# Kernel tuning notes

Hardware: AMD Instinct MI355X
Metric: run time of the kernel (lower is better)

## Reference

```python
import jax, jax.numpy as jnp
import numpy as np

D_MODEL = 2048
D_INNER = 4096
D_CONV = 4
D_STATE = 16
DT_RANK = 128  # (d_model + 15) // 16
EPS = 1e-5
B_SZ, SEQ = 2, 2048


def _silu(x):
    return x * jax.nn.sigmoid(x)


def setup_inputs() -> dict:
    key = jax.random.key(0)
    ks = jax.random.split(key, 10)
    s = lambda k, shape, sc=0.02: jax.random.normal(k, shape, jnp.float32) * sc
    # S4D-real init for A_log, small negative bias for dt (standard Mamba init)
    A_log = jnp.log(jnp.tile(jnp.arange(1, D_STATE + 1, dtype=jnp.float32), (D_INNER, 1)))
    return {
        "hidden_states": jax.random.normal(ks[0], (B_SZ, SEQ, D_MODEL), jnp.float32),
        "norm_scale": jnp.ones((D_MODEL,), jnp.float32),
        "in_proj_w": s(ks[1], (2 * D_INNER, D_MODEL)),
        "conv_w": s(ks[2], (D_INNER, 1, D_CONV), 0.1),
        "conv_b": s(ks[3], (D_INNER,), 0.1),
        "x_proj_w": s(ks[4], (DT_RANK + 2 * D_STATE, D_INNER)),
        "dt_proj_w": s(ks[5], (D_INNER, DT_RANK), 0.1),
        "dt_proj_b": jnp.full((D_INNER,), -4.0, jnp.float32) + s(ks[6], (D_INNER,), 0.1),
        "out_proj_w": s(ks[7], (D_MODEL, D_INNER)),
        "A_log": A_log,
        "D": jnp.ones((D_INNER,), jnp.float32),
    }


def reference(hidden_states, norm_scale, in_proj_w, conv_w, conv_b, x_proj_w,
              dt_proj_w, dt_proj_b, out_proj_w, A_log, D):
    B, L, _ = hidden_states.shape
    residual = hidden_states
    # RMSNorm
    rms = jnp.sqrt(jnp.mean(hidden_states ** 2, axis=-1, keepdims=True) + EPS)
    xn = hidden_states / rms * norm_scale
    # in_proj -> [B, L, 2*d_inner]; torch code keeps this as projected_states
    xz = jnp.einsum('bld,ed->ble', xn, in_proj_w)
    x_in = xz[..., :D_INNER].transpose(0, 2, 1)  # [B, d_inner, L]
    z = xz[..., D_INNER:]                        # [B, L, d_inner]
    # depthwise causal conv1d (padding d_conv-1, truncated to L) + SiLU
    xc = jax.lax.conv_general_dilated(
        x_in, conv_w, window_strides=(1,), padding=[(D_CONV - 1, 0)],
        feature_group_count=D_INNER)
    xc = _silu(xc + conv_b[None, :, None])       # [B, d_inner, L]
    # x_proj -> dt, B, C
    x_dbl = jnp.einsum('bdl,rd->brl', xc, x_proj_w)  # [B, dt_rank+2*d_state, L]
    dt_low = x_dbl[:, :DT_RANK]
    Bm = x_dbl[:, DT_RANK:DT_RANK + D_STATE]         # [B, d_state, L]
    Cm = x_dbl[:, DT_RANK + D_STATE:]                # [B, d_state, L]
    delta = jax.nn.softplus(
        jnp.einsum('dr,brl->bdl', dt_proj_w, dt_low) + dt_proj_b[None, :, None])
    A = -jnp.exp(A_log)                              # [d_inner, d_state]
    # selective scan: h_t = exp(delta_t * A) * h_{t-1} + delta_t * B_t * u_t
    delta_t = delta.transpose(2, 0, 1)  # [L, B, d_inner]
    u_t = xc.transpose(2, 0, 1)         # [L, B, d_inner]
    B_t = Bm.transpose(2, 0, 1)         # [L, B, d_state]
    C_t = Cm.transpose(2, 0, 1)         # [L, B, d_state]

    def step(h, inp):
        d_, b_, c_, u_ = inp
        dA = jnp.exp(d_[..., None] * A)                      # [B, d_inner, d_state]
        h = h * dA + (d_ * u_)[..., None] * b_[:, None, :]   # [B, d_inner, d_state]
        y = jnp.einsum('bds,bs->bd', h, c_)                  # [B, d_inner]
        return h, y

    h0 = jnp.zeros((B, D_INNER, D_STATE), hidden_states.dtype)
    _, ys = jax.lax.scan(step, h0, (delta_t, B_t, C_t, u_t))  # [L, B, d_inner]
    y = ys.transpose(1, 0, 2) + xc.transpose(0, 2, 1) * D     # [B, L, d_inner]
    y = y * _silu(z)
    out = jnp.einsum('bld,od->blo', y, out_proj_w)            # [B, L, d_model]
    return residual + out, xz
```

## Files before the change

### kernel.cpp

```cpp
#include <hip/hip_runtime.h>
#include <cstdint>
#include <cstddef>

#define DM   2048
#define DI   4096
#define DST  16
#define DTR  128
#define SEQL 2048
#define NTOK 4096
#define XZW  8192
#define NCHAIN 8192
#define CL   32
#define NCH  64

typedef short short8 __attribute__((ext_vector_type(8)));
typedef float f32x4 __attribute__((ext_vector_type(4)));

__device__ __forceinline__ short f2bf(float x) {
  union { float f; uint32_t u; } v; v.f = x;
  uint32_t r = v.u + 0x7fffu + ((v.u >> 16) & 1u);
  return (short)(r >> 16);
}
__device__ __forceinline__ float bf2f(short s) {
  union { uint32_t u; float f; } v; v.u = ((uint32_t)(uint16_t)s) << 16;
  return v.f;
}

__device__ __forceinline__ void stage16(const short* g, short* l) {
#if __has_builtin(__builtin_amdgcn_global_load_lds)
  __builtin_amdgcn_global_load_lds((const __attribute__((address_space(1))) void*)g,
                                   (__attribute__((address_space(3))) void*)l, 16, 0, 0);
#else
  *(short8*)l = *(const short8*)g;
#endif
}

__global__ __launch_bounds__(256) void cvt4_k(const float* __restrict__ in,
                                              short* __restrict__ out, int n4) {
  int i = blockIdx.x * 256 + threadIdx.x;
  if (i >= n4) return;
  float4 v = ((const float4*)in)[i];
  short4 o;
  o.x = f2bf(v.x); o.y = f2bf(v.y); o.z = f2bf(v.z); o.w = f2bf(v.w);
  ((short4*)out)[i] = o;
}

__global__ __launch_bounds__(256) void pad_xproj_k(const float* __restrict__ xp,
                                                   short* __restrict__ out) {
  int i = blockIdx.x * 256 + threadIdx.x;
  if (i >= 256 * 1024) return;
  int r = i >> 10;
  float4 v = make_float4(0.f, 0.f, 0.f, 0.f);
  if (r < 160) v = ((const float4*)xp)[i];
  short4 o;
  o.x = f2bf(v.x); o.y = f2bf(v.y); o.z = f2bf(v.z); o.w = f2bf(v.w);
  ((short4*)out)[i] = o;
}

__global__ __launch_bounds__(256) void rmsnorm_k(const float* __restrict__ hs,
                                                 const float* __restrict__ sc,
                                                 short* __restrict__ xn) {
  const int token = blockIdx.x;
  const int tid = threadIdx.x;
  const float* row = hs + (size_t)token * DM;
  float4 a = ((const float4*)row)[tid];
  float4 b = ((const float4*)row)[tid + 256];
  float ss = a.x*a.x + a.y*a.y + a.z*a.z + a.w*a.w
           + b.x*b.x + b.y*b.y + b.z*b.z + b.w*b.w;
  #pragma unroll
  for (int o = 32; o > 0; o >>= 1) ss += __shfl_xor(ss, o);
  __shared__ float wsum[4];
  if ((tid & 63) == 0) wsum[tid >> 6] = ss;
  __syncthreads();
  float tot = wsum[0] + wsum[1] + wsum[2] + wsum[3];
  float inv = rsqrtf(tot * (1.0f / DM) + 1e-5f);
  float4 s1 = ((const float4*)sc)[tid];
  float4 s2 = ((const float4*)sc)[tid + 256];
  short4 o1, o2;
  o1.x = f2bf(a.x * inv * s1.x); o1.y = f2bf(a.y * inv * s1.y);
  o1.z = f2bf(a.z * inv * s1.z); o1.w = f2bf(a.w * inv * s1.w);
  o2.x = f2bf(b.x * inv * s2.x); o2.y = f2bf(b.y * inv * s2.y);
  o2.z = f2bf(b.z * inv * s2.z); o2.w = f2bf(b.w * inv * s2.w);
  ((short4*)xn)[(size_t)token * (DM / 4) + tid] = o1;
  ((short4*)xn)[(size_t)token * (DM / 4) + tid + 256] = o2;
}

#define LGKM_FENCE() do { asm volatile("s_waitcnt lgkmcnt(0)" ::: "memory"); \
                          __builtin_amdgcn_sched_barrier(0); } while (0)

template <int RBY, int RBX>
__global__ __launch_bounds__(512) void gemm_big(const short* __restrict__ A,
                                                const short* __restrict__ B,
                                                int K, int ksz, int N, int nbx,
                                                float* __restrict__ out_f,
                                                size_t zstride) {
  constexpr int MFR = 8;
  constexpr int BM = 256;
  constexpr int ABYTES = BM * 128;
  constexpr int BBYTES = 256 * 128;
  constexpr int BUF = ABYTES + BBYTES;
  constexpr int FPP = 4;
  __shared__ char lds[2 * BUF];

  const int tid = threadIdx.x;
  const int lane = tid & 63;
  const int wid = tid >> 6;
  const int wm = wid >> 2;
  const int wn = wid & 3;
  const int lr = lane & 15;
  const int lj = lane >> 4;

  const int xcd = blockIdx.x & 7;
  const int idx = blockIdx.x >> 3;
  const int nrgx = nbx / RBX;
  const int by = (xcd / nrgx) * RBY + idx / RBX;
  const int bx = (xcd % nrgx) * RBX + idx % RBX;
  const size_t m0 = (size_t)by * BM;
  const size_t n0 = (size_t)bx * 256;

  const int kbase = blockIdx.y * ksz;
  out_f += (size_t)blockIdx.y * zstride;
  const int NT = ksz >> 6;

  auto stA1 = [&](int t, char* buf, int s) {
    const int k0 = kbase + (t << 6);
    const int off = s * 8192 + tid * 16;
    const int r = off >> 7;
    const int j = (off >> 4) & 7;
    stage16(A + (m0 + r) * (size_t)K + k0 + ((j ^ (r & 7)) << 3),
            (short*)(buf + off));
  };
  auto stB1 = [&](int t, char* buf, int s) {
    const int k0 = kbase + (t << 6);
    const int off = s * 8192 + tid * 16;
    const int r = off >> 7;
    const int j = (off >> 4) & 7;
    stage16(B + (n0 + r) * (size_t)K + k0 + ((j ^ (r & 7)) << 3),
            (short*)(buf + ABYTES + off));
  };

#define READ_A(dst, fbase)                                                   \
  _Pragma("unroll")                                                          \
  for (int f = 0; f < 4; ++f) {                                              \
    const int arow = wm * (BM / 2) + ((fbase) + f) * 16 + lr;                \
    _Pragma("unroll")                                                        \
    for (int ks = 0; ks < 2; ++ks)                                           \
      dst[f][ks] = *(const short8*)(cur + arow * 128 +                       \
                     ((((ks << 2) + lj) ^ (arow & 7)) << 4));                \
  }
#define READ_B(dst, gbase)                                                   \
  _Pragma("unroll")                                                          \
  for (int g = 0; g < 2; ++g) {                                              \
    const int brow = wn * 64 + ((gbase) + g) * 16 + lr;                      \
    _Pragma("unroll")                                                        \
    for (int ks = 0; ks < 2; ++ks)                                           \
      dst[g][ks] = *(const short8*)(cur + ABYTES + brow * 128 +              \
                     ((((ks << 2) + lj) ^ (brow & 7)) << 4));                \
  }
#define MFMA_Q(accoff, avoff, gbase, bvx)                                    \
  __builtin_amdgcn_s_setprio(1);                                             \
  _Pragma("unroll")                                                          \
  for (int ks = 0; ks < 2; ++ks)                                             \
    _Pragma("unroll")                                                        \
    for (int f = 0; f < FPP; ++f)                                            \
      _Pragma("unroll")                                                      \
      for (int g = 0; g < 2; ++g)                                            \
        acc[(accoff) + f][(gbase) + g] = __builtin_amdgcn_mfma_f32_16x16x32_bf16( \
            av[(avoff) + f][ks], bvx[g][ks], acc[(accoff) + f][(gbase) + g], 0, 0, 0); \
  __builtin_amdgcn_s_setprio(0);

  f32x4 acc[MFR][4] = {};

  {
    #pragma unroll
    for (int s = 0; s < 4; ++s) stA1(0, lds, s);
    #pragma unroll
    for (int s = 0; s < 4; ++s) stB1(0, lds, s);
    if (NT > 1) {
      stA1(1, lds + BUF, 0); stA1(1, lds + BUF, 2);
      asm volatile("s_waitcnt vmcnt(2)" ::: "memory");
    } else asm volatile("s_waitcnt vmcnt(0)" ::: "memory");
    __builtin_amdgcn_s_barrier();
    __builtin_amdgcn_sched_barrier(0);
  }

  for (int t = 0; t < NT; ++t) {
    char* cur = lds + (t & 1) * BUF;
    char* nxt = lds + ((t + 1) & 1) * BUF;
    const bool m1 = (t + 1) < NT;
    const bool m2 = (t + 2) < NT;
    short8 av[4][2], bv0[2][2], bv1[2][2];

    READ_A(av, 0);
    READ_B(bv0, 0);
    if (m1) { stA1(t + 1, nxt, 1); stA1(t + 1, nxt, 3); }
    LGKM_FENCE();
    MFMA_Q(0, 0, 0, bv0);
    __builtin_amdgcn_s_barrier();

    READ_B(bv1, 2);
    if (m1) { stB1(t + 1, nxt, 0); stB1(t + 1, nxt, 1); }
    LGKM_FENCE();
    MFMA_Q(0, 0, 2, bv1);
    __builtin_amdgcn_s_barrier();

    READ_A(av, 4);
    if (m1) { stB1(t + 1, nxt, 2); stB1(t + 1, nxt, 3); }
    if (m2) { stA1(t + 2, cur, 0); stA1(t + 2, cur, 2); }
    LGKM_FENCE();
    MFMA_Q(4, 0, 2, bv1);
    __builtin_amdgcn_s_barrier();

    MFMA_Q(4, 0, 0, bv0);
    if (m2) asm volatile("s_waitcnt vmcnt(2)" ::: "memory");
    else    asm volatile("s_waitcnt vmcnt(0)" ::: "memory");
    __builtin_amdgcn_s_barrier();
    __builtin_amdgcn_sched_barrier(0);
  }

  #pragma unroll
  for (int f = 0; f < MFR; ++f)
    #pragma unroll
    for (int g = 0; g < 4; ++g)
      #pragma unroll
      for (int jj = 0; jj < 4; ++jj) {
        const size_t row = m0 + wm * (BM / 2) + f * 16 + lj * 4 + jj;
        const size_t col = n0 + wn * 64 + g * 16 + lr;
        out_f[row * (size_t)N + col] = acc[f][g][jj];
      }
#undef READ_A
#undef READ_B
#undef MFMA_Q
}

__global__ __launch_bounds__(256) void combine_k(const float* __restrict__ part,
                                                 const float* __restrict__ hs,
                                                 float* __restrict__ out0) {
  const size_t i = (size_t)blockIdx.x * 256 + threadIdx.x;
  const float4 p0 = ((const float4*)part)[i];
  const float4 p1 = ((const float4*)part)[i + (size_t)NTOK * DM / 4];
  const float4 r  = ((const float4*)hs)[i];
  float4 o;
  o.x = r.x + p0.x + p1.x; o.y = r.y + p0.y + p1.y;
  o.z = r.z + p0.z + p1.z; o.w = r.w + p0.w + p1.w;
  ((float4*)out0)[i] = o;
}

template <int EPI>
__global__ __launch_bounds__(256) void gemm_nt(const short* __restrict__ A,
                                               const short* __restrict__ B,
                                               int ld, int K, int N,
                                               float* __restrict__ out_f,
                                               const float* __restrict__ aux_f,
                                               short* __restrict__ out_bf) {
  __shared__ short As[128 * 64];
  __shared__ short Bs[128 * 64];
  const int tid = threadIdx.x;
  const int lane = tid & 63;
  const int wid = tid >> 6;
  const int wr = wid >> 1, wc = wid & 1;
  const size_t m0 = (size_t)blockIdx.y * 128;
  const size_t n0 = (size_t)blockIdx.x * 128;
  A += (size_t)blockIdx.z * K;
  B += (size_t)blockIdx.z * K;
  f32x4 acc[4][4] = {};
  for (int k0 = 0; k0 < K; k0 += 64) {
    #pragma unroll
    for (int i = 0; i < 4; ++i) {
      const int off = i * 4096 + tid * 16;
      const int r = off >> 7;
      const int ke = (off & 127) >> 1;
      stage16(A + (m0 + r) * (size_t)ld + k0 + ke, &As[off >> 1]);
      stage16(B + (n0 + r) * (size_t)ld + k0 + ke, &Bs[off >> 1]);
    }
    __syncthreads();
    #pragma unroll
    for (int kk = 0; kk < 64; kk += 32) {
      short8 af[4], bfr[4];
      const int kb = kk + (lane >> 4) * 8;
      const int rr = lane & 15;
      #pragma unroll
      for (int f = 0; f < 4; ++f) {
        af[f]  = *(const short8*)&As[(wr * 64 + f * 16 + rr) * 64 + kb];
        bfr[f] = *(const short8*)&Bs[(wc * 64 + f * 16 + rr) * 64 + kb];
      }
      #pragma unroll
      for (int fm = 0; fm < 4; ++fm)
        #pragma unroll
        for (int fn = 0; fn < 4; ++fn)
          acc[fm][fn] = __builtin_amdgcn_mfma_f32_16x16x32_bf16(af[fm], bfr[fn], acc[fm][fn], 0, 0, 0);
    }
    __syncthreads();
  }
  const int rbase = (lane >> 4) * 4;
  const int cbase = lane & 15;
  #pragma unroll
  for (int fm = 0; fm < 4; ++fm) {
    #pragma unroll
    for (int fn = 0; fn < 4; ++fn) {
      #pragma unroll
      for (int j = 0; j < 4; ++j) {
        const size_t row = m0 + wr * 64 + fm * 16 + rbase + j;
        const size_t col = n0 + wc * 64 + fn * 16 + cbase;
        const float v = acc[fm][fn][j];
        if constexpr (EPI == 2) {
          float x = v + aux_f[col];
          float sp = (x > 20.f) ? x : log1pf(__expf(x));
          out_bf[row * (size_t)N + col] = f2bf(sp);
        } else {
          if (col < 160)
            out_f[((size_t)blockIdx.z * NTOK + row) * (size_t)N + col] = v;
        }
      }
    }
  }
}

__global__ __launch_bounds__(256) void xdbl_epi_k(const float* __restrict__ part,
                                                  short* __restrict__ dtl,
                                                  float* __restrict__ Bc,
                                                  float* __restrict__ Cc) {
  const int row = blockIdx.x;
  const int col = threadIdx.x;
  if (col >= 160) return;
  const size_t i = (size_t)row * 256 + col;
  const float v = part[i] + part[(size_t)NTOK * 256 + i]
                + part[(size_t)2 * NTOK * 256 + i]
                + part[(size_t)3 * NTOK * 256 + i];
  if (col < 128)      dtl[(size_t)row * 128 + col] = f2bf(v);
  else if (col < 144) Bc[(size_t)row * 16 + (col - 128)] = v;
  else                Cc[(size_t)row * 16 + (col - 144)] = v;
}

__global__ __launch_bounds__(256) void conv_silu_k(const float* __restrict__ xz,
                                                   const float* __restrict__ cw,
                                                   const float* __restrict__ cb,
                                                   short* __restrict__ xc) {
  const int d = blockIdx.x * 256 + threadIdx.x;
  const int t0 = blockIdx.y * 8;
  const int l0 = t0 & (SEQL - 1);
  const float4 w = ((const float4*)cw)[d];
  const float bias = cb[d];
  float x0 = (l0 >= 3) ? xz[(size_t)(t0 - 3) * XZW + d] : 0.f;
  float x1 = (l0 >= 2) ? xz[(size_t)(t0 - 2) * XZW + d] : 0.f;
  float x2 = (l0 >= 1) ? xz[(size_t)(t0 - 1) * XZW + d] : 0.f;
  #pragma unroll
  for (int i = 0; i < 8; ++i) {
    const float x3 = xz[(size_t)(t0 + i) * XZW + d];
    const float acc = bias + w.x * x0 + w.y * x1 + w.z * x2 + w.w * x3;
    const float sv = acc / (1.f + __expf(-acc));
    xc[(size_t)(t0 + i) * DI + d] = f2bf(sv);
    x0 = x1; x1 = x2; x2 = x3;
  }
}

__global__ __launch_bounds__(256) void scan1_k(const short* __restrict__ del_bf,
                                               const short* __restrict__ xc,
                                               const float* __restrict__ Bc,
                                               const float* __restrict__ alog,
                                               float* __restrict__ hloc,
                                               float* __restrict__ Ssum) {
  const int t = blockIdx.x * 256 + threadIdx.x;
  const int sub = t & 1;
  const int chain = (t >> 1) & (NCHAIN - 1);
  const int chunk = t >> 14;
  const int b = chain >> 12;
  const int d = chain & 4095;
  float A[8];
  #pragma unroll
  for (int j = 0; j < 8; ++j) A[j] = -__expf(alog[d * 16 + sub * 8 + j]);
  float h[8] = {};
  float S = 0.f;
  size_t token = (size_t)b * SEQL + (size_t)chunk * CL;
  #pragma unroll 2
  for (int l = 0; l < CL; ++l, ++token) {
    const float delta = bf2f(del_bf[token * DI + d]);
    const float u = bf2f(xc[token * DI + d]);
    const float du = delta * u;
    S += delta;
    const float4 B0 = ((const float4*)Bc)[token * 4 + sub * 2];
    const float4 B1 = ((const float4*)Bc)[token * 4 + sub * 2 + 1];
    const float Bv[8] = {B0.x, B0.y, B0.z, B0.w, B1.x, B1.y, B1.z, B1.w};
    #pragma unroll
    for (int j = 0; j < 8; ++j)
      h[j] = h[j] * __expf(delta * A[j]) + du * Bv[j];
  }
  const size_t idx = (size_t)(chunk * NCHAIN + chain) * 4 + sub * 2;
  ((float4*)hloc)[idx]     = make_float4(h[0], h[1], h[2], h[3]);
  ((float4*)hloc)[idx + 1] = make_float4(h[4], h[5], h[6], h[7]);
  if (sub == 0) Ssum[chunk * NCHAIN + chain] = S;
}

__global__ __launch_bounds__(256) void scan2_k(float* __restrict__ hloc,
                                               const float* __restrict__ Ssum,
                                               const float* __restrict__ alog) {
  const int t = blockIdx.x * 256 + threadIdx.x;
  const int q = t & 3;
  const int chain = t >> 2;
  const int d = chain & 4095;
  float A[4];
  #pragma unroll
  for (int j = 0; j < 4; ++j) A[j] = -__expf(alog[d * 16 + q * 4 + j]);
  float4 h = make_float4(0.f, 0.f, 0.f, 0.f);
  for (int c = 0; c < NCH; ++c) {
    const size_t idx = (size_t)(c * NCHAIN + chain) * 4 + q;
    const float S = Ssum[c * NCHAIN + chain];
    const float4 hl = ((const float4*)hloc)[idx];
    ((float4*)hloc)[idx] = h;
    h.x = h.x * __expf(A[0] * S) + hl.x;
    h.y = h.y * __expf(A[1] * S) + hl.y;
    h.z = h.z * __expf(A[2] * S) + hl.z;
    h.w = h.w * __expf(A[3] * S) + hl.w;
  }
}

__global__ __launch_bounds__(256) void scan3_k(const short* __restrict__ del_bf,
                                               const short* __restrict__ xc,
                                               const float* __restrict__ Bc,
                                               const float* __restrict__ Cc,
                                               const float* __restrict__ xzbuf,
                                               const float* __restrict__ alog,
                                               const float* __restrict__ dvec,
                                               const float* __restrict__ hin,
                                               short* __restrict__ y) {
  const int t = blockIdx.x * 256 + threadIdx.x;
  const int sub = t & 1;
  const int chain = (t >> 1) & (NCHAIN - 1);
  const int chunk = t >> 14;
  const int b = chain >> 12;
  const int d = chain & 4095;
  float A[8];
  #pragma unroll
  for (int j = 0; j < 8; ++j) A[j] = -__expf(alog[d * 16 + sub * 8 + j]);
  const float Dd = dvec[d];
  const size_t idx = (size_t)(chunk * NCHAIN + chain) * 4 + sub * 2;
  const float4 h0 = ((const float4*)hin)[idx];
  const float4 h1 = ((const float4*)hin)[idx + 1];
  float h[8] = {h0.x, h0.y, h0.z, h0.w, h1.x, h1.y, h1.z, h1.w};
  size_t token = (size_t)b * SEQL + (size_t)chunk * CL;
  #pragma unroll 2
  for (int l = 0; l < CL; ++l, ++token) {
    const float delta = bf2f(del_bf[token * DI + d]);
    const float u = bf2f(xc[token * DI + d]);
    const float du = delta * u;
    const float4 B0 = ((const float4*)Bc)[token * 4 + sub * 2];
    const float4 B1 = ((const float4*)Bc)[token * 4 + sub * 2 + 1];
    const float4 C0 = ((const float4*)Cc)[token * 4 + sub * 2];
    const float4 C1 = ((const float4*)Cc)[token * 4 + sub * 2 + 1];
    const float Bv[8] = {B0.x, B0.y, B0.z, B0.w, B1.x, B1.y, B1.z, B1.w};
    const float Cv[8] = {C0.x, C0.y, C0.z, C0.w, C1.x, C1.y, C1.z, C1.w};
    float yp = 0.f;
    #pragma unroll
    for (int j = 0; j < 8; ++j) {
      h[j] = h[j] * __expf(delta * A[j]) + du * Bv[j];
      yp += h[j] * Cv[j];
    }
    yp += __shfl_xor(yp, 1);
    if (sub == 0) {
      const float z = xzbuf[token * XZW + DI + d];
      const float sz = z / (1.f + __expf(-z));
      y[token * DI + d] = f2bf((yp + u * Dd) * sz);
    }
  }
}

extern "C" void kernel_launch(void* const* d_in, const int* in_sizes, int n_in,
                              void* d_out, int out_size, void* d_ws, size_t ws_size,
                              hipStream_t stream) {
  const float* hs   = (const float*)d_in[0];
  const float* nsc  = (const float*)d_in[1];
  const float* win  = (const float*)d_in[2];
  const float* cw   = (const float*)d_in[3];
  const float* cb   = (const float*)d_in[4];
  const float* wxp  = (const float*)d_in[5];
  const float* wdt  = (const float*)d_in[6];
  const float* bdt  = (const float*)d_in[7];
  const float* wout = (const float*)d_in[8];
  const float* alog = (const float*)d_in[9];
  const float* dvec = (const float*)d_in[10];

  float* out0 = (float*)d_out;
  float* xz   = out0 + (size_t)NTOK * DM;

  char* w = (char*)d_ws;
  size_t off = 0;
  auto alloc = [&](size_t bytes) {
    char* p = w + off;
    off += (bytes + 255) & ~(size_t)255;
    return p;
  };
  short* xn_bf   = (short*)alloc((size_t)NTOK * DM * 2);
  short* win_bf  = (short*)alloc((size_t)XZW * DM * 2);
  short* wout_bf = (short*)alloc((size_t)DM * DI * 2);
  short* wdt_bf  = (short*)alloc((size_t)DI * DTR * 2);
  short* wxp_bf  = (short*)alloc((size_t)256 * DI * 2);
  short* xc_bf   = (short*)alloc((size_t)NTOK * DI * 2);
  short* dtl_bf  = (short*)alloc((size_t)NTOK * DTR * 2);
  float* Bc      = (float*)alloc((size_t)NTOK * DST * 4);
  float* Cc      = (float*)alloc((size_t)NTOK * DST * 4);
  short* del_bf  = (short*)alloc((size_t)NTOK * DI * 2);
  short* y_bf    = (short*)alloc((size_t)NTOK * DI * 2);

  float* xp_part = (float*)win_bf;
  float* hloc    = (float*)win_bf;
  float* Ssum    = (float*)xn_bf;
  float* opart   = (float*)xc_bf;

  cvt4_k<<<16384, 256, 0, stream>>>(win,  win_bf,  (XZW * DM) / 4);
  cvt4_k<<<8192,  256, 0, stream>>>(wout, wout_bf, (DM * DI) / 4);
  cvt4_k<<<512,   256, 0, stream>>>(wdt,  wdt_bf,  (DI * DTR) / 4);
  pad_xproj_k<<<1024, 256, 0, stream>>>(wxp, wxp_bf);

  rmsnorm_k<<<NTOK, 256, 0, stream>>>(hs, nsc, xn_bf);
  gemm_big<8, 8><<<dim3((XZW / 256) * (NTOK / 256)), 512, 0, stream>>>(
      xn_bf, win_bf, DM, DM, XZW, XZW / 256, xz, 0);
  conv_silu_k<<<dim3(DI / 256, NTOK / 8), 256, 0, stream>>>(xz, cw, cb, xc_bf);
  gemm_nt<4><<<dim3(2, NTOK / 128, 4), 256, 0, stream>>>(
      xc_bf, wxp_bf, DI, DI / 4, 256, xp_part, nullptr, nullptr);
  xdbl_epi_k<<<NTOK, 256, 0, stream>>>(xp_part, dtl_bf, Bc, Cc);
  gemm_nt<2><<<dim3(DI / 128, NTOK / 128, 1), 256, 0, stream>>>(
      dtl_bf, wdt_bf, DTR, DTR, DI, nullptr, bdt, del_bf);
  scan1_k<<<(NCHAIN * 2 * NCH) / 256, 256, 0, stream>>>(
      del_bf, xc_bf, Bc, alog, hloc, Ssum);
  scan2_k<<<(NCHAIN * 4) / 256, 256, 0, stream>>>(hloc, Ssum, alog);
  scan3_k<<<(NCHAIN * 2 * NCH) / 256, 256, 0, stream>>>(
      del_bf, xc_bf, Bc, Cc, xz, alog, dvec, hloc, y_bf);
  gemm_big<4, 4><<<dim3((DM / 256) * (NTOK / 256), 2), 512, 0, stream>>>(
      y_bf, wout_bf, DI, DI / 2, DM, DM / 256, opart, (size_t)NTOK * DM);
  combine_k<<<(NTOK * DM / 4) / 256, 256, 0, stream>>>(opart, hs, out0);
}
```

Measured before the change: 560.6 us.

## Rework big GEMM prefetch schedule, permute B tile rows, and merge weight converts

The big GEMM now stages the entire next K-tile in the prologue and spreads the t+2 prefetch across the four phases of each iteration, with extra barriers and adjusted vmcnt/lgkmcnt waits. B rows are permuted in LDS so each wave's two B-fragment halves come from contiguous 128-row blocks. The four weight-conversion launches are merged into one kernel. The intent is better overlap of global loads with MFMA work and fewer launches, at the cost of more barriers per iteration and more complex wait counts that could stall or race if miscounted.

```diff
diff --git a/kernel.cpp b/kernel.cpp
--- a/kernel.cpp
+++ b/kernel.cpp
@@ -35,26 +35,41 @@
 #endif
 }
 
-__global__ __launch_bounds__(256) void cvt4_k(const float* __restrict__ in,
-                                              short* __restrict__ out, int n4) {
-  int i = blockIdx.x * 256 + threadIdx.x;
-  if (i >= n4) return;
-  float4 v = ((const float4*)in)[i];
+#define NG_WIN  (XZW * DM / 4)
+#define NG_WOUT (DM * DI / 4)
+#define NG_WDT  (DI * DTR / 4)
+#define NG_PAD  (256 * DI / 4)
+__global__ __launch_bounds__(256) void wcvt_k(const float* __restrict__ win,
+                                              const float* __restrict__ wout,
+                                              const float* __restrict__ wdt,
+                                              const float* __restrict__ xp,
+                                              short* __restrict__ win_bf,
+                                              short* __restrict__ wout_bf,
+                                              short* __restrict__ wdt_bf,
+                                              short* __restrict__ wxp_bf) {
+  const size_t i = (size_t)blockIdx.x * 256 + threadIdx.x;
+  float4 v;
+  short4* dst;
+  if (i < NG_WIN) {
+    v = ((const float4*)win)[i];
+    dst = (short4*)win_bf + i;
+  } else if (i < NG_WIN + NG_WOUT) {
+    const size_t j = i - NG_WIN;
+    v = ((const float4*)wout)[j];
+    dst = (short4*)wout_bf + j;
+  } else if (i < NG_WIN + NG_WOUT + NG_WDT) {
+    const size_t j = i - NG_WIN - NG_WOUT;
+    v = ((const float4*)wdt)[j];
+    dst = (short4*)wdt_bf + j;
+  } else {
+    const size_t j = i - NG_WIN - NG_WOUT - NG_WDT;
+    const int r = (int)(j >> 10);
+    v = (r < 160) ? ((const float4*)xp)[j] : make_float4(0.f, 0.f, 0.f, 0.f);
+    dst = (short4*)wxp_bf + j;
+  }
   short4 o;
   o.x = f2bf(v.x); o.y = f2bf(v.y); o.z = f2bf(v.z); o.w = f2bf(v.w);
-  ((short4*)out)[i] = o;
-}
-
-__global__ __launch_bounds__(256) void pad_xproj_k(const float* __restrict__ xp,
-                                                   short* __restrict__ out) {
-  int i = blockIdx.x * 256 + threadIdx.x;
-  if (i >= 256 * 1024) return;
-  int r = i >> 10;
-  float4 v = make_float4(0.f, 0.f, 0.f, 0.f);
-  if (r < 160) v = ((const float4*)xp)[i];
-  short4 o;
-  o.x = f2bf(v.x); o.y = f2bf(v.y); o.z = f2bf(v.z); o.w = f2bf(v.w);
-  ((short4*)out)[i] = o;
+  *dst = o;
 }
 
 __global__ __launch_bounds__(256) void rmsnorm_k(const float* __restrict__ hs,
@@ -99,7 +114,6 @@
   constexpr int ABYTES = BM * 128;
   constexpr int BBYTES = 256 * 128;
   constexpr int BUF = ABYTES + BBYTES;
-  constexpr int FPP = 4;
   __shared__ char lds[2 * BUF];
 
   const int tid = threadIdx.x;
@@ -133,16 +147,18 @@
   auto stB1 = [&](int t, char* buf, int s) {
     const int k0 = kbase + (t << 6);
     const int off = s * 8192 + tid * 16;
-    const int r = off >> 7;
+    const int q = off >> 7;
     const int j = (off >> 4) & 7;
-    stage16(B + (n0 + r) * (size_t)K + k0 + ((j ^ (r & 7)) << 3),
+    const int grow = (q < 128) ? ((q >> 5) * 64 + (q & 31))
+                               : (((q - 128) >> 5) * 64 + 32 + ((q - 128) & 31));
+    stage16(B + (n0 + grow) * (size_t)K + k0 + ((j ^ (q & 7)) << 3),
             (short*)(buf + ABYTES + off));
   };
 
 #define READ_A(dst, fbase)                                                   \
   _Pragma("unroll")                                                          \
   for (int f = 0; f < 4; ++f) {                                              \
-    const int arow = wm * (BM / 2) + ((fbase) + f) * 16 + lr;                \
+    const int arow = wm * 128 + ((fbase) + f) * 16 + lr;                     \
     _Pragma("unroll")                                                        \
     for (int ks = 0; ks < 2; ++ks)                                           \
       dst[f][ks] = *(const short8*)(cur + arow * 128 +                       \
@@ -151,22 +167,22 @@
 #define READ_B(dst, gbase)                                                   \
   _Pragma("unroll")                                                          \
   for (int g = 0; g < 2; ++g) {                                              \
-    const int brow = wn * 64 + ((gbase) + g) * 16 + lr;                      \
+    const int q = ((gbase) >= 2 ? 128 : 0) + (wn << 5) + g * 16 + lr;        \
     _Pragma("unroll")                                                        \
     for (int ks = 0; ks < 2; ++ks)                                           \
-      dst[g][ks] = *(const short8*)(cur + ABYTES + brow * 128 +              \
-                     ((((ks << 2) + lj) ^ (brow & 7)) << 4));                \
-  }
-#define MFMA_Q(accoff, avoff, gbase, bvx)                                    \
+      dst[g][ks] = *(const short8*)(cur + ABYTES + q * 128 +                 \
+                     ((((ks << 2) + lj) ^ (q & 7)) << 4));                   \
+  }
+#define MFMA_Q(accoff, gbase, bvx)                                           \
   __builtin_amdgcn_s_setprio(1);                                             \
   _Pragma("unroll")                                                          \
   for (int ks = 0; ks < 2; ++ks)                                             \
     _Pragma("unroll")                                                        \
-    for (int f = 0; f < FPP; ++f)                                            \
+    for (int f = 0; f < 4; ++f)                                              \
       _Pragma("unroll")                                                      \
       for (int g = 0; g < 2; ++g)                                            \
         acc[(accoff) + f][(gbase) + g] = __builtin_amdgcn_mfma_f32_16x16x32_bf16( \
-            av[(avoff) + f][ks], bvx[g][ks], acc[(accoff) + f][(gbase) + g], 0, 0, 0); \
+            av[f][ks], bvx[g][ks], acc[(accoff) + f][(gbase) + g], 0, 0, 0); \
   __builtin_amdgcn_s_setprio(0);
 
   f32x4 acc[MFR][4] = {};
@@ -177,42 +193,49 @@
     #pragma unroll
     for (int s = 0; s < 4; ++s) stB1(0, lds, s);
     if (NT > 1) {
-      stA1(1, lds + BUF, 0); stA1(1, lds + BUF, 2);
-      asm volatile("s_waitcnt vmcnt(2)" ::: "memory");
-    } else asm volatile("s_waitcnt vmcnt(0)" ::: "memory");
+      #pragma unroll
+      for (int s = 0; s < 4; ++s) stA1(1, lds + BUF, s);
+      #pragma unroll
+      for (int s = 0; s < 4; ++s) stB1(1, lds + BUF, s);
+      asm volatile("s_waitcnt vmcnt(8)" ::: "memory");
+    } else {
+      asm volatile("s_waitcnt vmcnt(0)" ::: "memory");
+    }
     __builtin_amdgcn_s_barrier();
     __builtin_amdgcn_sched_barrier(0);
   }
 
   for (int t = 0; t < NT; ++t) {
     char* cur = lds + (t & 1) * BUF;
-    char* nxt = lds + ((t + 1) & 1) * BUF;
-    const bool m1 = (t + 1) < NT;
     const bool m2 = (t + 2) < NT;
     short8 av[4][2], bv0[2][2], bv1[2][2];
 
     READ_A(av, 0);
     READ_B(bv0, 0);
-    if (m1) { stA1(t + 1, nxt, 1); stA1(t + 1, nxt, 3); }
+    asm volatile("s_waitcnt lgkmcnt(8)" ::: "memory");
+    __builtin_amdgcn_s_barrier();
     LGKM_FENCE();
-    MFMA_Q(0, 0, 0, bv0);
+    MFMA_Q(0, 0, bv0);
     __builtin_amdgcn_s_barrier();
 
     READ_B(bv1, 2);
-    if (m1) { stB1(t + 1, nxt, 0); stB1(t + 1, nxt, 1); }
+    if (m2) { stA1(t + 2, cur, 0); stA1(t + 2, cur, 2);
+              stB1(t + 2, cur, 0); stB1(t + 2, cur, 1); }
+    __builtin_amdgcn_s_barrier();
     LGKM_FENCE();
-    MFMA_Q(0, 0, 2, bv1);
+    MFMA_Q(0, 2, bv1);
     __builtin_amdgcn_s_barrier();
 
     READ_A(av, 4);
-    if (m1) { stB1(t + 1, nxt, 2); stB1(t + 1, nxt, 3); }
-    if (m2) { stA1(t + 2, cur, 0); stA1(t + 2, cur, 2); }
+    if (m2) { stB1(t + 2, cur, 2); stB1(t + 2, cur, 3); }
+    __builtin_amdgcn_s_barrier();
     LGKM_FENCE();
-    MFMA_Q(4, 0, 2, bv1);
-    __builtin_amdgcn_s_barrier();
-
-    MFMA_Q(4, 0, 0, bv0);
-    if (m2) asm volatile("s_waitcnt vmcnt(2)" ::: "memory");
+    MFMA_Q(4, 2, bv1);
+    __builtin_amdgcn_s_barrier();
+
+    if (m2) { stA1(t + 2, cur, 1); stA1(t + 2, cur, 3); }
+    MFMA_Q(4, 0, bv0);
+    if (m2) asm volatile("s_waitcnt vmcnt(6)" ::: "memory");
     else    asm volatile("s_waitcnt vmcnt(0)" ::: "memory");
     __builtin_amdgcn_s_barrier();
     __builtin_amdgcn_sched_barrier(0);
@@ -224,7 +247,7 @@
     for (int g = 0; g < 4; ++g)
       #pragma unroll
       for (int jj = 0; jj < 4; ++jj) {
-        const size_t row = m0 + wm * (BM / 2) + f * 16 + lj * 4 + jj;
+        const size_t row = m0 + wm * 128 + f * 16 + lj * 4 + jj;
         const size_t col = n0 + wn * 64 + g * 16 + lr;
         out_f[row * (size_t)N + col] = acc[f][g][jj];
       }
@@ -506,10 +529,8 @@
   float* Ssum    = (float*)xn_bf;
   float* opart   = (float*)xc_bf;
 
-  cvt4_k<<<16384, 256, 0, stream>>>(win,  win_bf,  (XZW * DM) / 4);
-  cvt4_k<<<8192,  256, 0, stream>>>(wout, wout_bf, (DM * DI) / 4);
-  cvt4_k<<<512,   256, 0, stream>>>(wdt,  wdt_bf,  (DI * DTR) / 4);
-  pad_xproj_k<<<1024, 256, 0, stream>>>(wxp, wxp_bf);
+  wcvt_k<<<(NG_WIN + NG_WOUT + NG_WDT + NG_PAD) / 256, 256, 0, stream>>>(
+      win, wout, wdt, wxp, win_bf, wout_bf, wdt_bf, wxp_bf);
 
   rmsnorm_k<<<NTOK, 256, 0, stream>>>(hs, nsc, xn_bf);
   gemm_big<8, 8><<<dim3((XZW / 256) * (NTOK / 256)), 512, 0, stream>>>(
```

New measurement: 570.6 us. Within noise of the previous version (+1.8%).
